# Kernel tuning notes

Hardware: AMD Instinct MI355X
Metric: run time of the kernel (lower is better)

## Reference

```python
import jax, jax.numpy as jnp
import numpy as np

HEAD = 8

def setup_inputs() -> dict:
    key = jax.random.key(0)
    k1, k2 = jax.random.split(key)
    B, S, D = 4, 2048, 512
    x = jax.random.normal(k1, (B, S, D), dtype=jnp.float32)
    Wq = jax.random.normal(k2, (D, D), dtype=jnp.float32) * (1.0 / np.sqrt(D))
    return {"x": x, "Wq": Wq}


def reference(x, Wq):
    # Faithful to source: Q, K, V all use linear_q (bug preserved).
    B, S, D = x.shape
    hd = D // HEAD
    q = jnp.einsum('bsd,de->bse', x, Wq)
    # Q = K = V = q
    qh = q.reshape(B, S, HEAD, hd).transpose(0, 2, 1, 3)  # [B,H,S,hd]
    # scale by sqrt(head_dim): inputs.shape[-1] inside ScaleDotAttentionLayer
    scores = jnp.einsum('bhqd,bhkd->bhqk', qh, qh) / jnp.sqrt(jnp.float32(hd))
    weights = jax.nn.softmax(scores, axis=-1)
    ctx = jnp.einsum('bhqk,bhkd->bhqd', weights, qh)
    out = ctx.transpose(0, 2, 1, 3).reshape(B, S, D)
    return out
```

## Files before the change

### kernel.cpp

```cpp
#include <hip/hip_runtime.h>
#include <hip/hip_fp16.h>
#include <math.h>

#define SS 2048
#define DD 512
#define NH 8
#define HD 64

typedef __attribute__((ext_vector_type(8))) short frag_ab;
typedef __attribute__((ext_vector_type(4))) float frag_cd;
typedef __attribute__((ext_vector_type(4))) _Float16 frag_b4;

static __device__ inline unsigned int pack_h2(float x, float y) {
    __half2 t = __floats2half2_rn(x, y);
    return *(unsigned int*)&t;
}

__global__ __launch_bounds__(256, 4) void gemm_kernel(const float* __restrict__ x,
                                                      const float* __restrict__ w,
                                                      unsigned short* __restrict__ q) {
    __shared__ __align__(16) unsigned short Ah[2][64 * 72];
    __shared__ __align__(16) unsigned short Bt[2][64 * 72];
    const int tid = threadIdx.x;
    const int lane = tid & 63, wv = tid >> 6;
    const int a = lane & 15, g = lane >> 4;
    const int bm = blockIdx.x, bn = blockIdx.y;

    frag_cd acc[4] = {};
    const int asr = tid >> 4;
    const int ac4 = (tid & 15) * 4;
    const int bnn = (tid & 31) * 2;
    const int bkk = (tid >> 5) * 8;

    float4 av[4];
    float2 bv[8];
    #pragma unroll
    for (int p = 0; p < 4; ++p)
        av[p] = *(const float4*)(x + (size_t)(bm * 64 + asr + p * 16) * 512 + ac4);
    #pragma unroll
    for (int j = 0; j < 8; ++j)
        bv[j] = *(const float2*)(w + (size_t)(bkk + j) * 512 + bn * 64 + bnn);

    for (int it = 0; it < 8; ++it) {
        const int cur = it & 1;
        #pragma unroll
        for (int p = 0; p < 4; ++p) {
            uint2 hh = { pack_h2(av[p].x, av[p].y), pack_h2(av[p].z, av[p].w) };
            *(uint2*)&Ah[cur][(asr + p * 16) * 72 + ac4] = hh;
        }
        {
            unsigned int t0[4], t1[4];
            #pragma unroll
            for (int j = 0; j < 4; ++j) {
                t0[j] = pack_h2(bv[2 * j].x, bv[2 * j + 1].x);
                t1[j] = pack_h2(bv[2 * j].y, bv[2 * j + 1].y);
            }
            *(uint4*)&Bt[cur][bnn * 72 + bkk]       = *(uint4*)t0;
            *(uint4*)&Bt[cur][(bnn + 1) * 72 + bkk] = *(uint4*)t1;
        }
        __syncthreads();
        if (it < 7) {
            const int k0 = (it + 1) * 64;
            #pragma unroll
            for (int p = 0; p < 4; ++p)
                av[p] = *(const float4*)(x + (size_t)(bm * 64 + asr + p * 16) * 512 + k0 + ac4);
            #pragma unroll
            for (int j = 0; j < 8; ++j)
                bv[j] = *(const float2*)(w + (size_t)(k0 + bkk + j) * 512 + bn * 64 + bnn);
        }
        #pragma unroll
        for (int kh = 0; kh < 2; ++kh) {
            const frag_ab bf = *(const frag_ab*)&Bt[cur][(wv * 16 + a) * 72 + kh * 32 + g * 8];
            #pragma unroll
            for (int mt = 0; mt < 4; ++mt) {
                const frag_ab af = *(const frag_ab*)&Ah[cur][(mt * 16 + a) * 72 + kh * 32 + g * 8];
                acc[mt] = __builtin_amdgcn_mfma_f32_16x16x32_f16(af, bf, acc[mt], 0, 0, 0);
            }
        }
    }
    #pragma unroll
    for (int mt = 0; mt < 4; ++mt)
        #pragma unroll
        for (int r = 0; r < 4; ++r) {
            const int m = bm * 64 + mt * 16 + g * 4 + r;
            const int n = bn * 64 + wv * 16 + a;
            __half hv = __float2half_rn(acc[mt][r]);
            q[(size_t)m * 512 + n] = *(unsigned short*)&hv;
        }
}

__global__ __launch_bounds__(512, 4) void attn_kernel(const __half* __restrict__ qg,
                                                      float* __restrict__ out) {
    __shared__ __align__(16) unsigned char LDSB[34816];
    unsigned short* KtB = (unsigned short*)LDSB;
    unsigned short* VtB = (unsigned short*)(LDSB + 18432);

    const int tid = threadIdx.x;
    const int lane = tid & 63, wv = tid >> 6;
    const int a = lane & 15, g = lane >> 4;
    const int qq = wv & 3;
    const int kv = wv >> 2;
    const int bid = blockIdx.x;
    const int qt = bid & 15;
    const int h  = (bid >> 4) & 7;
    const int b  = bid >> 7;

    const unsigned short* qbh = (const unsigned short*)qg + (size_t)b * SS * DD + h * HD;
    const int qrow0 = qt * 128 + qq * 32;

    frag_ab qf[2][2];
    const __half2 qsc = __float2half2_rn(0.18033688011112042f);
    #pragma unroll
    for (int nt = 0; nt < 2; ++nt)
        #pragma unroll
        for (int kh = 0; kh < 2; ++kh) {
            frag_ab t = *(const frag_ab*)(qbh + (size_t)(qrow0 + nt * 16 + a) * DD + kh * 32 + g * 8);
            __half2* phh = (__half2*)&t;
            #pragma unroll
            for (int i = 0; i < 4; ++i) phh[i] = __hmul2(phh[i], qsc);
            qf[nt][kh] = t;
        }

    frag_cd oacc[4][2] = {};
    float lsum[2] = {0.f, 0.f};

    const int t8 = tid & 255;
    const int f0 = (t8 & 31) * 2;
    const int u8 = t8 >> 5;
    const int r0 = u8 * 8;
    const int keybase = (tid >> 8) * 1024;
    unsigned short* Ks = KtB + (tid >> 8) * 4608;
    unsigned short* Vs = VtB + (tid >> 8) * 4096;
    const int vsw = (u8 ^ (t8 & 7)) << 3;

    unsigned int d[8];
    #pragma unroll
    for (int k = 0; k < 8; ++k)
        d[k] = *(const unsigned int*)(qbh + (size_t)(keybase + r0 + k) * DD + f0);

    const unsigned short* Kc = KtB + kv * 4608;
    const unsigned short* Vc = VtB + kv * 4096;
    const float coff = -11.541560327111707f;
    const int sv = (a >> 1) & 7;

    for (int it = 0; it < 16; ++it) {
        __syncthreads();
        #pragma unroll
        for (int k = 0; k < 8; ++k)
            *(unsigned int*)&Ks[(r0 + k) * 72 + f0] = d[k];
        {
            unsigned int vlo[4], vhi[4];
            #pragma unroll
            for (int j = 0; j < 4; ++j) {
                vlo[j] = (d[2 * j] & 0xFFFFu) | (d[2 * j + 1] << 16);
                vhi[j] = (d[2 * j] >> 16)     | (d[2 * j + 1] & 0xFFFF0000u);
            }
            *(uint4*)&Vs[f0 * 64 + vsw]       = *(uint4*)vlo;
            *(uint4*)&Vs[(f0 + 1) * 64 + vsw] = *(uint4*)vhi;
        }
        __syncthreads();

        if (it + 1 < 16) {
            const int kb = keybase + (it + 1) * 64;
            #pragma unroll
            for (int k = 0; k < 8; ++k)
                d[k] = *(const unsigned int*)(qbh + (size_t)(kb + r0 + k) * DD + f0);
        }

        #pragma unroll
        for (int kt = 0; kt < 4; ++kt) {
            const frag_ab ka0 = *(const frag_ab*)&Kc[(kt * 16 + a) * 72 + g * 8];
            const frag_ab ka1 = *(const frag_ab*)&Kc[(kt * 16 + a) * 72 + 32 + g * 8];
            frag_b4 pbk[2];
            #pragma unroll
            for (int nt = 0; nt < 2; ++nt) {
                frag_cd c = {coff, coff, coff, coff};
                c = __builtin_amdgcn_mfma_f32_16x16x32_f16(ka0, qf[nt][0], c, 0, 0, 0);
                c = __builtin_amdgcn_mfma_f32_16x16x32_f16(ka1, qf[nt][1], c, 0, 0, 0);
                const float p0 = __builtin_amdgcn_exp2f(c[0]);
                const float p1 = __builtin_amdgcn_exp2f(c[1]);
                const float p2 = __builtin_amdgcn_exp2f(c[2]);
                const float p3 = __builtin_amdgcn_exp2f(c[3]);
                lsum[nt] += (p0 + p1) + (p2 + p3);
                union { unsigned int u[2]; frag_b4 h; } pu;
                pu.u[0] = pack_h2(p0, p1);
                pu.u[1] = pack_h2(p2, p3);
                pbk[nt] = pu.h;
            }
            const int vch = ((2 * kt + (g >> 1)) ^ sv) << 3;
            const int vof = (g & 1) << 2;
            #pragma unroll
            for (int ft = 0; ft < 4; ++ft) {
                const frag_b4 va = *(const frag_b4*)&Vc[(ft * 16 + a) * 64 + vch + vof];
                oacc[ft][0] = __builtin_amdgcn_mfma_f32_16x16x16f16(va, pbk[0], oacc[ft][0], 0, 0, 0);
                oacc[ft][1] = __builtin_amdgcn_mfma_f32_16x16x16f16(va, pbk[1], oacc[ft][1], 0, 0, 0);
            }
        }
    }

    #pragma unroll
    for (int nt = 0; nt < 2; ++nt) {
        lsum[nt] += __shfl_xor(lsum[nt], 16, 64);
        lsum[nt] += __shfl_xor(lsum[nt], 32, 64);
    }
    __syncthreads();
    float* Obuf = (float*)LDSB;
    float* Lbuf = (float*)(LDSB + 33792);
    if (kv == 1) {
        #pragma unroll
        for (int ft = 0; ft < 4; ++ft)
            #pragma unroll
            for (int nt = 0; nt < 2; ++nt)
                #pragma unroll
                for (int r = 0; r < 4; ++r)
                    Obuf[qq * 2112 + (ft * 16 + g * 4 + r) * 33 + nt * 16 + a] = oacc[ft][nt][r];
        if (g == 0)
            #pragma unroll
            for (int nt = 0; nt < 2; ++nt)
                Lbuf[qq * 32 + nt * 16 + a] = lsum[nt];
    }
    __syncthreads();
    if (kv == 0) {
        #pragma unroll
        for (int nt = 0; nt < 2; ++nt) {
            const float inv = 1.f / (lsum[nt] + Lbuf[qq * 32 + nt * 16 + a]);
            float* op = out + ((size_t)b * SS + qrow0 + nt * 16 + a) * DD + h * HD;
            #pragma unroll
            for (int ft = 0; ft < 4; ++ft) {
                const int fb = ft * 16 + g * 4;
                float4 vv = {
                    (oacc[ft][nt][0] + Obuf[qq * 2112 + (fb + 0) * 33 + nt * 16 + a]) * inv,
                    (oacc[ft][nt][1] + Obuf[qq * 2112 + (fb + 1) * 33 + nt * 16 + a]) * inv,
                    (oacc[ft][nt][2] + Obuf[qq * 2112 + (fb + 2) * 33 + nt * 16 + a]) * inv,
                    (oacc[ft][nt][3] + Obuf[qq * 2112 + (fb + 3) * 33 + nt * 16 + a]) * inv };
                *(float4*)(op + fb) = vv;
            }
        }
    }
}

extern "C" void kernel_launch(void* const* d_in, const int* in_sizes, int n_in,
                              void* d_out, int out_size, void* d_ws, size_t ws_size,
                              hipStream_t stream) {
    const float* x  = (const float*)d_in[0];
    const float* wq = (const float*)d_in[1];
    float* out = (float*)d_out;
    unsigned short* q_h = (unsigned short*)d_ws;

    dim3 ggrid(128, 8);
    gemm_kernel<<<ggrid, 256, 0, stream>>>(x, wq, q_h);
    attn_kernel<<<512, 512, 0, stream>>>((const __half*)q_h, out);
}
```

Before: 126.5 us.

## Double-buffer attention K/V in LDS and enlarge GEMM tiles to 128x128

The attention kernel now keeps two LDS buffers for K/V and writes the next tile while computing on the current one, so each iteration needs one barrier instead of two. This doubles its LDS use to about 68 KB per block, which may cut how many blocks fit on a CU. The GEMM moves to 128x128 tiles on 512 threads, with 8 waves each computing a 64x32 sub-tile, and a restructured prefetch/stage pipeline. The goal is more operand reuse and fewer barriers, at the price of more registers and fewer blocks.

After: 122.6 us. 1.03x faster.

```diff
diff --git a/kernel.cpp b/kernel.cpp
--- a/kernel.cpp
+++ b/kernel.cpp
@@ -16,84 +16,97 @@
     return *(unsigned int*)&t;
 }
 
-__global__ __launch_bounds__(256, 4) void gemm_kernel(const float* __restrict__ x,
+__global__ __launch_bounds__(512, 2) void gemm_kernel(const float* __restrict__ x,
                                                       const float* __restrict__ w,
                                                       unsigned short* __restrict__ q) {
-    __shared__ __align__(16) unsigned short Ah[2][64 * 72];
-    __shared__ __align__(16) unsigned short Bt[2][64 * 72];
+    __shared__ __align__(16) unsigned short Ah[2][128 * 72];
+    __shared__ __align__(16) unsigned short Bt[2][128 * 72];
     const int tid = threadIdx.x;
     const int lane = tid & 63, wv = tid >> 6;
     const int a = lane & 15, g = lane >> 4;
     const int bm = blockIdx.x, bn = blockIdx.y;
-
-    frag_cd acc[4] = {};
-    const int asr = tid >> 4;
-    const int ac4 = (tid & 15) * 4;
-    const int bnn = (tid & 31) * 2;
-    const int bkk = (tid >> 5) * 8;
+    const int wr = wv >> 2, wc = wv & 3;
+
+    frag_cd acc[4][2] = {};
+    const int ar = tid >> 2;
+    const int ak = (tid & 3) * 16;
+    const int bnn = (tid & 63) * 2;
+    const int bkk = (tid >> 6) * 8;
 
     float4 av[4];
     float2 bv[8];
-    #pragma unroll
-    for (int p = 0; p < 4; ++p)
-        av[p] = *(const float4*)(x + (size_t)(bm * 64 + asr + p * 16) * 512 + ac4);
-    #pragma unroll
-    for (int j = 0; j < 8; ++j)
-        bv[j] = *(const float2*)(w + (size_t)(bkk + j) * 512 + bn * 64 + bnn);
+
+    auto load_tiles = [&](int k0) {
+        #pragma unroll
+        for (int i = 0; i < 4; ++i)
+            av[i] = *(const float4*)(x + (size_t)(bm * 128 + ar) * 512 + k0 + ak + 4 * i);
+        #pragma unroll
+        for (int j = 0; j < 8; ++j)
+            bv[j] = *(const float2*)(w + (size_t)(k0 + bkk + j) * 512 + bn * 128 + bnn);
+    };
+    auto stage_tiles = [&](int buf) {
+        unsigned int ha[8];
+        #pragma unroll
+        for (int i = 0; i < 4; ++i) {
+            ha[2 * i]     = pack_h2(av[i].x, av[i].y);
+            ha[2 * i + 1] = pack_h2(av[i].z, av[i].w);
+        }
+        *(uint4*)&Ah[buf][ar * 72 + ak]     = *(uint4*)&ha[0];
+        *(uint4*)&Ah[buf][ar * 72 + ak + 8] = *(uint4*)&ha[4];
+        unsigned int t0[4], t1[4];
+        #pragma unroll
+        for (int j = 0; j < 4; ++j) {
+            t0[j] = pack_h2(bv[2 * j].x, bv[2 * j + 1].x);
+            t1[j] = pack_h2(bv[2 * j].y, bv[2 * j + 1].y);
+        }
+        *(uint4*)&Bt[buf][bnn * 72 + bkk]       = *(uint4*)t0;
+        *(uint4*)&Bt[buf][(bnn + 1) * 72 + bkk] = *(uint4*)t1;
+    };
+
+    load_tiles(0);
+    stage_tiles(0);
+    load_tiles(64);
+    __syncthreads();
 
     for (int it = 0; it < 8; ++it) {
         const int cur = it & 1;
-        #pragma unroll
-        for (int p = 0; p < 4; ++p) {
-            uint2 hh = { pack_h2(av[p].x, av[p].y), pack_h2(av[p].z, av[p].w) };
-            *(uint2*)&Ah[cur][(asr + p * 16) * 72 + ac4] = hh;
-        }
-        {
-            unsigned int t0[4], t1[4];
-            #pragma unroll
-            for (int j = 0; j < 4; ++j) {
-                t0[j] = pack_h2(bv[2 * j].x, bv[2 * j + 1].x);
-                t1[j] = pack_h2(bv[2 * j].y, bv[2 * j + 1].y);
-            }
-            *(uint4*)&Bt[cur][bnn * 72 + bkk]       = *(uint4*)t0;
-            *(uint4*)&Bt[cur][(bnn + 1) * 72 + bkk] = *(uint4*)t1;
+        if (it < 7) stage_tiles(cur ^ 1);
+        if (it < 6) load_tiles((it + 2) * 64);
+        #pragma unroll
+        for (int kh = 0; kh < 2; ++kh) {
+            frag_ab bf[2], af[4];
+            #pragma unroll
+            for (int nt = 0; nt < 2; ++nt)
+                bf[nt] = *(const frag_ab*)&Bt[cur][(wc * 32 + nt * 16 + a) * 72 + kh * 32 + g * 8];
+            #pragma unroll
+            for (int mt = 0; mt < 4; ++mt)
+                af[mt] = *(const frag_ab*)&Ah[cur][(wr * 64 + mt * 16 + a) * 72 + kh * 32 + g * 8];
+            #pragma unroll
+            for (int mt = 0; mt < 4; ++mt)
+                #pragma unroll
+                for (int nt = 0; nt < 2; ++nt)
+                    acc[mt][nt] = __builtin_amdgcn_mfma_f32_16x16x32_f16(af[mt], bf[nt], acc[mt][nt], 0, 0, 0);
         }
         __syncthreads();
-        if (it < 7) {
-            const int k0 = (it + 1) * 64;
-            #pragma unroll
-            for (int p = 0; p < 4; ++p)
-                av[p] = *(const float4*)(x + (size_t)(bm * 64 + asr + p * 16) * 512 + k0 + ac4);
-            #pragma unroll
-            for (int j = 0; j < 8; ++j)
-                bv[j] = *(const float2*)(w + (size_t)(k0 + bkk + j) * 512 + bn * 64 + bnn);
-        }
-        #pragma unroll
-        for (int kh = 0; kh < 2; ++kh) {
-            const frag_ab bf = *(const frag_ab*)&Bt[cur][(wv * 16 + a) * 72 + kh * 32 + g * 8];
-            #pragma unroll
-            for (int mt = 0; mt < 4; ++mt) {
-                const frag_ab af = *(const frag_ab*)&Ah[cur][(mt * 16 + a) * 72 + kh * 32 + g * 8];
-                acc[mt] = __builtin_amdgcn_mfma_f32_16x16x32_f16(af, bf, acc[mt], 0, 0, 0);
-            }
-        }
     }
     #pragma unroll
     for (int mt = 0; mt < 4; ++mt)
         #pragma unroll
-        for (int r = 0; r < 4; ++r) {
-            const int m = bm * 64 + mt * 16 + g * 4 + r;
-            const int n = bn * 64 + wv * 16 + a;
-            __half hv = __float2half_rn(acc[mt][r]);
-            q[(size_t)m * 512 + n] = *(unsigned short*)&hv;
-        }
+        for (int nt = 0; nt < 2; ++nt)
+            #pragma unroll
+            for (int r = 0; r < 4; ++r) {
+                const int m = bm * 128 + wr * 64 + mt * 16 + g * 4 + r;
+                const int n = bn * 128 + wc * 32 + nt * 16 + a;
+                __half hv = __float2half_rn(acc[mt][nt][r]);
+                q[(size_t)m * 512 + n] = *(unsigned short*)&hv;
+            }
 }
 
 __global__ __launch_bounds__(512, 4) void attn_kernel(const __half* __restrict__ qg,
                                                       float* __restrict__ out) {
-    __shared__ __align__(16) unsigned char LDSB[34816];
+    __shared__ __align__(16) unsigned char LDSB[69632];
     unsigned short* KtB = (unsigned short*)LDSB;
-    unsigned short* VtB = (unsigned short*)(LDSB + 18432);
+    unsigned short* VtB = (unsigned short*)(LDSB + 36864);
 
     const int tid = threadIdx.x;
     const int lane = tid & 63, wv = tid >> 6;
@@ -129,8 +142,8 @@
     const int u8 = t8 >> 5;
     const int r0 = u8 * 8;
     const int keybase = (tid >> 8) * 1024;
-    unsigned short* Ks = KtB + (tid >> 8) * 4608;
-    unsigned short* Vs = VtB + (tid >> 8) * 4096;
+    unsigned short* KsBase = KtB + (tid >> 8) * 4608;
+    unsigned short* VsBase = VtB + (tid >> 8) * 4096;
     const int vsw = (u8 ^ (t8 & 7)) << 3;
 
     unsigned int d[8];
@@ -138,34 +151,44 @@
     for (int k = 0; k < 8; ++k)
         d[k] = *(const unsigned int*)(qbh + (size_t)(keybase + r0 + k) * DD + f0);
 
-    const unsigned short* Kc = KtB + kv * 4608;
-    const unsigned short* Vc = VtB + kv * 4096;
+    const unsigned short* KcBase = KtB + kv * 4608;
+    const unsigned short* VcBase = VtB + kv * 4096;
     const float coff = -11.541560327111707f;
     const int sv = (a >> 1) & 7;
 
+    auto stage_write = [&](int buf) {
+        unsigned short* Ksb = KsBase + buf * 9216;
+        unsigned short* Vsb = VsBase + buf * 8192;
+        #pragma unroll
+        for (int k = 0; k < 8; ++k)
+            *(unsigned int*)&Ksb[(r0 + k) * 72 + f0] = d[k];
+        unsigned int vlo[4], vhi[4];
+        #pragma unroll
+        for (int j = 0; j < 4; ++j) {
+            vlo[j] = (d[2 * j] & 0xFFFFu) | (d[2 * j + 1] << 16);
+            vhi[j] = (d[2 * j] >> 16)     | (d[2 * j + 1] & 0xFFFF0000u);
+        }
+        *(uint4*)&Vsb[f0 * 64 + vsw]       = *(uint4*)vlo;
+        *(uint4*)&Vsb[(f0 + 1) * 64 + vsw] = *(uint4*)vhi;
+    };
+
+    stage_write(0);
+    #pragma unroll
+    for (int k = 0; k < 8; ++k)
+        d[k] = *(const unsigned int*)(qbh + (size_t)(keybase + 64 + r0 + k) * DD + f0);
+    __syncthreads();
+
     for (int it = 0; it < 16; ++it) {
-        __syncthreads();
-        #pragma unroll
-        for (int k = 0; k < 8; ++k)
-            *(unsigned int*)&Ks[(r0 + k) * 72 + f0] = d[k];
-        {
-            unsigned int vlo[4], vhi[4];
-            #pragma unroll
-            for (int j = 0; j < 4; ++j) {
-                vlo[j] = (d[2 * j] & 0xFFFFu) | (d[2 * j + 1] << 16);
-                vhi[j] = (d[2 * j] >> 16)     | (d[2 * j + 1] & 0xFFFF0000u);
-            }
-            *(uint4*)&Vs[f0 * 64 + vsw]       = *(uint4*)vlo;
-            *(uint4*)&Vs[(f0 + 1) * 64 + vsw] = *(uint4*)vhi;
-        }
-        __syncthreads();
-
-        if (it + 1 < 16) {
-            const int kb = keybase + (it + 1) * 64;
+        const int cur = it & 1;
+        if (it < 15) stage_write(cur ^ 1);
+        if (it < 14) {
+            const int kb = keybase + (it + 2) * 64;
             #pragma unroll
             for (int k = 0; k < 8; ++k)
                 d[k] = *(const unsigned int*)(qbh + (size_t)(kb + r0 + k) * DD + f0);
         }
+        const unsigned short* Kc = KcBase + cur * 9216;
+        const unsigned short* Vc = VcBase + cur * 8192;
 
         #pragma unroll
         for (int kt = 0; kt < 4; ++kt) {
@@ -196,6 +219,7 @@
                 oacc[ft][1] = __builtin_amdgcn_mfma_f32_16x16x16f16(va, pbk[1], oacc[ft][1], 0, 0, 0);
             }
         }
+        __syncthreads();
     }
 
     #pragma unroll
@@ -203,7 +227,6 @@
         lsum[nt] += __shfl_xor(lsum[nt], 16, 64);
         lsum[nt] += __shfl_xor(lsum[nt], 32, 64);
     }
-    __syncthreads();
     float* Obuf = (float*)LDSB;
     float* Lbuf = (float*)(LDSB + 33792);
     if (kv == 1) {
@@ -247,7 +270,7 @@
     float* out = (float*)d_out;
     unsigned short* q_h = (unsigned short*)d_ws;
 
-    dim3 ggrid(128, 8);
-    gemm_kernel<<<ggrid, 256, 0, stream>>>(x, wq, q_h);
+    dim3 ggrid(64, 4);
+    gemm_kernel<<<ggrid, 512, 0, stream>>>(x, wq, q_h);
     attn_kernel<<<512, 512, 0, stream>>>((const __half*)q_h, out);
 }
```
